# Kernel tuning notes

Hardware: AMD Instinct MI355X
Metric: run time of the kernel (lower is better)

The kernel has to match this reference:

```python
import jax, jax.numpy as jnp
import numpy as np
from jax import lax

MAX_W = 4           # max_subword_block_width
DOWNSAMPLE = 2      # downsample_rate


def setup_inputs() -> dict:
    key = jax.random.key(0)
    k1, k2, k3, k4 = jax.random.split(key, 4)
    B, E, L, K = 8, 512, 4096, 5
    x = jax.random.normal(k1, (B, E, L), dtype=jnp.float32)
    conv_w = jax.random.normal(k2, (E, E, K), dtype=jnp.float32) * (1.0 / np.sqrt(E * K))
    conv_b = jax.random.normal(k3, (E,), dtype=jnp.float32) * 0.02
    score_w = jax.random.normal(k4, (E,), dtype=jnp.float32) * (1.0 / np.sqrt(E))
    return {"x": x, "conv_w": conv_w, "conv_b": conv_b, "score_w": score_w}


def reference(x, conv_w, conv_b, score_w):
    B, E, L = x.shape  # `length` captured BEFORE conv, as in the torch code
    # pre-GBST conv, VALID padding: length becomes L - K + 1
    y = lax.conv_general_dilated(
        x, conv_w, window_strides=(1,), padding='VALID',
        dimension_numbers=('NCH', 'OIH', 'NCH')) + conv_b[None, :, None]
    L2 = y.shape[-1]
    seqs, scores = [], []
    for w in range(1, MAX_W + 1):
        pad = (-L2) % w
        yp = jnp.pad(y, ((0, 0), (0, 0), (0, pad)))  # zero-pad to multiple of w
        nb = yp.shape[-1] // w
        pooled = yp.reshape(B, E, nb, w).mean(-1)          # avg_pool1d(kernel=w, stride=w)
        sc = jnp.einsum('ben,e->bn', pooled, score_w)      # Linear(E,1,bias=False)
        rs = jnp.repeat(pooled, w, axis=-1)                # repeat_interleave
        rsc = jnp.repeat(sc, w, axis=-1)
        cur = rs.shape[-1]
        if cur < L:  # re-pad with zeros up to the ORIGINAL (pre-conv) length
            rs = jnp.pad(rs, ((0, 0), (0, 0), (0, L - cur)))
            rsc = jnp.pad(rsc, ((0, 0), (0, L - cur)))
        seqs.append(rs[:, :, :L])
        scores.append(rsc[:, :L])
    S = jnp.stack(seqs, axis=-1)                           # [B,E,L,W]
    A = jax.nn.softmax(jnp.stack(scores, axis=-1), axis=-1)  # [B,L,W]
    out = jnp.einsum('belw,blw->bel', S, A)                # softmax-weighted combine
    r = DOWNSAMPLE
    Ld = (L // r) * r
    out = out[:, :, :Ld].reshape(B, E, L // r, r).mean(-1)  # final avg_pool1d
    return out
```

## Files before the change

kernel.cpp:

```cpp
#include <hip/hip_runtime.h>
#include <stdint.h>

#define E_DIM 512
#define L_IN  4096
#define L_OUT 4092
#define KW    5
#define B_DIM 8
#define L2P   4096
#define L_DS  2048
#define LP    4160

typedef __attribute__((ext_vector_type(8))) short short8;
typedef __attribute__((ext_vector_type(4))) float f32x4;

__device__ __forceinline__ unsigned short f2bf(float f) {
    uint32_t u = __float_as_uint(f);
    u += 0x7fffu + ((u >> 16) & 1);
    return (unsigned short)(u >> 16);
}
__device__ __forceinline__ float bf2f(unsigned short h) {
    return __uint_as_float((uint32_t)h << 16);
}

__global__ __launch_bounds__(256)
void xt_kernel(const float* __restrict__ x, unsigned short* __restrict__ Xt)
{
    const int b  = blockIdx.z;
    const int i0 = blockIdx.y * 64;
    const int l0 = blockIdx.x * 64;
    __shared__ float T[64][65];
    const int tid = threadIdx.x;

    const int ir = tid >> 4;
    const int cq = (tid & 15) * 4;
    #pragma unroll
    for (int jj = 0; jj < 4; ++jj) {
        int i = jj * 16 + ir;
        float4 v = make_float4(0.f, 0.f, 0.f, 0.f);
        if (l0 < L_IN)
            v = *reinterpret_cast<const float4*>(
                &x[((size_t)b * E_DIM + i0 + i) * L_IN + l0 + cq]);
        T[i][cq + 0] = v.x; T[i][cq + 1] = v.y;
        T[i][cq + 2] = v.z; T[i][cq + 3] = v.w;
    }
    __syncthreads();
    const int h  = tid & 31;
    const int rq = tid >> 5;
    #pragma unroll
    for (int j = 0; j < 8; ++j) {
        int lr = j * 8 + rq;
        ushort2 o;
        o.x = f2bf(T[2 * h][lr]);
        o.y = f2bf(T[2 * h + 1][lr]);
        *reinterpret_cast<ushort2*>(
            &Xt[((size_t)b * LP + l0 + lr) * E_DIM + i0 + 2 * h]) = o;
    }
}

__global__ __launch_bounds__(256)
void wt_kernel(const float* __restrict__ w, unsigned short* __restrict__ Wt)
{
    int idx = blockIdx.x * 256 + threadIdx.x;
    if (idx >= E_DIM * E_DIM) return;
    #pragma unroll
    for (int k = 0; k < KW; ++k)
        Wt[(size_t)k * E_DIM * E_DIM + idx] = f2bf(w[(size_t)idx * KW + k]);
}

#define XS_ROWS  272
#define XS_BYTES (XS_ROWS * 64)
#define N_XCH    (XS_BYTES / 1024)
#define WS_OFF   XS_BYTES
#define WS_BYTES (5 * 128 * 64)
#define LDS_BYTES (XS_BYTES + WS_BYTES)
#define N_CH     (LDS_BYTES / 1024)

__global__ __launch_bounds__(256, 2)
void conv_mfma(const unsigned short* __restrict__ Xt,
               const unsigned short* __restrict__ Wt,
               const float* __restrict__ bias,
               const float* __restrict__ sw,
               unsigned short* __restrict__ y,
               float* __restrict__ sp)
{
    __shared__ __align__(16) unsigned char lds[LDS_BYTES];
    const int l0 = blockIdx.x * 256;
    const int e0 = blockIdx.y * 128;
    const int b  = blockIdx.z;
    const int tid  = threadIdx.x;
    const int lane = tid & 63;
    const int wv   = tid >> 6;
    const int wr = wv >> 1, wc = wv & 1;
    const int lr = lane & 15, lg = lane >> 4;
    const int ln4r = lane >> 2;
    const int xswz = ((lane & 3) ^ ((lane >> 3) & 3)) * 8;

    const int aBase = WS_OFF + (wr * 64 + lr) * 64
                    + ((lg ^ ((lr >> 1) & 3)) << 4);
    int bBase[KW];
    #pragma unroll
    for (int kt = 0; kt < KW; ++kt)
        bBase[kt] = (wc * 128 + lr + kt) * 64
                  + ((lg ^ (((lr + kt) >> 1) & 3)) << 4);

    f32x4 acc[4][8] = {};

    for (int ks = 0; ks < 16; ++ks) {
        const int i0 = ks * 32;
        __syncthreads();
        for (int cch = wv; cch < N_CH; cch += 4) {
            void* lp = (void*)(lds + cch * 1024);
            const unsigned short* gp;
            if (cch < N_XCH) {
                int row = cch * 16 + ln4r;
                gp = Xt + ((size_t)b * LP + l0 + row) * E_DIM + i0 + xswz;
            } else {
                int rk = (cch - N_XCH) * 16 + ln4r;
                int k = rk >> 7, er = rk & 127;
                gp = Wt + ((size_t)k * E_DIM + e0 + er) * E_DIM + i0 + xswz;
            }
            __builtin_amdgcn_global_load_lds(
                (const __attribute__((address_space(1))) void*)gp,
                (__attribute__((address_space(3))) void*)lp,
                16, 0, 0);
        }
        __syncthreads();
        #pragma unroll
        for (int kt = 0; kt < KW; ++kt) {
            short8 aF[4], bF[8];
            #pragma unroll
            for (int m = 0; m < 4; ++m)
                aF[m] = *reinterpret_cast<const short8*>(
                    &lds[aBase + (kt * 128 + m * 16) * 64]);
            #pragma unroll
            for (int n = 0; n < 8; ++n)
                bF[n] = *reinterpret_cast<const short8*>(
                    &lds[bBase[kt] + n * 1024]);
            #pragma unroll
            for (int m = 0; m < 4; ++m)
                #pragma unroll
                for (int n = 0; n < 8; ++n)
                    acc[m][n] = __builtin_amdgcn_mfma_f32_16x16x32_bf16(
                        aF[m], bF[n], acc[m][n], 0, 0, 0);
        }
    }

    float spn[8] = {};
    #pragma unroll
    for (int m = 0; m < 4; ++m)
        #pragma unroll
        for (int q = 0; q < 4; ++q) {
            int e = e0 + wr * 64 + m * 16 + lg * 4 + q;
            float bv = bias[e];
            float wv_s = sw[e];
            unsigned short* yr =
                y + ((size_t)b * E_DIM + e) * L2P + l0 + wc * 128 + lr;
            #pragma unroll
            for (int n = 0; n < 8; ++n) {
                float v = acc[m][n][q] + bv;
                yr[n * 16] = f2bf(v);
                spn[n] = fmaf(v, wv_s, spn[n]);
            }
        }
    #pragma unroll
    for (int n = 0; n < 8; ++n) {
        float p = spn[n];
        p += __shfl_xor(p, 16);
        p += __shfl_xor(p, 32);
        if (lane < 16) {
            int l = l0 + wc * 128 + n * 16 + lane;
            sp[((size_t)b * L2P + l) * 8 + blockIdx.y * 2 + wr] = p;
        }
    }
}

__global__ __launch_bounds__(256)
void weight_kernel(const float* __restrict__ sp, float* __restrict__ A)
{
    const int b  = blockIdx.y;
    const int l0 = blockIdx.x * 256;
    const int tid = threadIdx.x;
    __shared__ float sl[260];

    for (int idx = tid; idx < 260; idx += 256) {
        int l = l0 - 2 + idx;
        float v = 0.f;
        if (l >= 0 && l < L_OUT) {
            const float* p = &sp[((size_t)b * L2P + l) * 8];
            v = ((p[0] + p[1]) + (p[2] + p[3])) + ((p[4] + p[5]) + (p[6] + p[7]));
        }
        sl[idx] = v;
    }
    __syncthreads();

    const int l = l0 + tid;
    if (l >= L_OUT) return;
    #define SL(i) sl[(i) - (l0 - 2)]
    float sc0 = SL(l);
    int n2 = l & ~1;
    float sc1 = 0.5f * (SL(n2) + SL(n2 + 1));
    int n3 = (l / 3) * 3;
    float sc2 = (1.f / 3.f) * (SL(n3) + SL(n3 + 1) + SL(n3 + 2));
    int n4 = l & ~3;
    float sc3 = 0.25f * (SL(n4) + SL(n4 + 1) + SL(n4 + 2) + SL(n4 + 3));
    #undef SL

    float m  = fmaxf(fmaxf(sc0, sc1), fmaxf(sc2, sc3));
    float e0 = __expf(sc0 - m), e1 = __expf(sc1 - m);
    float e2 = __expf(sc2 - m), e3 = __expf(sc3 - m);
    float inv = 1.f / (e0 + e1 + e2 + e3);

    float4 av = make_float4(e0 * inv, e1 * inv, e2 * inv, e3 * inv);
    *reinterpret_cast<float4*>(&A[((size_t)b * L2P + l) * 4]) = av;
}

typedef __attribute__((ext_vector_type(8))) unsigned short u16x8;

__global__ __launch_bounds__(256)
void combine_kernel(const unsigned short* __restrict__ y,
                    const float* __restrict__ A, float* __restrict__ out)
{
    const int e = blockIdx.x;
    const int b = blockIdx.y;
    const int tid = threadIdx.x;
    __shared__ float ys[L2P];

    const unsigned short* yrow = y + ((size_t)b * E_DIM + e) * L2P;
    #pragma unroll
    for (int j = 0; j < 2; ++j) {
        int base = (tid + j * 256) * 8;
        u16x8 v = *reinterpret_cast<const u16x8*>(&yrow[base]);
        #pragma unroll
        for (int t = 0; t < 8; ++t) ys[base + t] = bf2f(v[t]);
    }
    __syncthreads();

    const float* Ab = A + (size_t)b * L2P * 4;
    float* orow = out + ((size_t)b * E_DIM + e) * L_DS;
    #pragma unroll
    for (int j = 0; j < 8; ++j) {
        int m = tid + j * 256;
        float acc = 0.f;
        #pragma unroll
        for (int r = 0; r < 2; ++r) {
            int l = 2 * m + r;
            if (l < L_OUT) {
                const float4 a4 = *reinterpret_cast<const float4*>(&Ab[l * 4]);
                float t = a4.x * ys[l];
                int n2 = l & ~1;
                t += a4.y * 0.5f * (ys[n2] + ys[n2 + 1]);
                int n3 = (l / 3) * 3;
                t += a4.z * (1.f / 3.f) * (ys[n3] + ys[n3 + 1] + ys[n3 + 2]);
                int n4 = l & ~3;
                t += a4.w * 0.25f * (ys[n4] + ys[n4 + 1] + ys[n4 + 2] + ys[n4 + 3]);
                acc += t;
            }
        }
        orow[m] = 0.5f * acc;
    }
}

extern "C" void kernel_launch(void* const* d_in, const int* in_sizes, int n_in,
                              void* d_out, int out_size, void* d_ws, size_t ws_size,
                              hipStream_t stream)
{
    const float* x  = (const float*)d_in[0];
    const float* w  = (const float*)d_in[1];
    const float* bb = (const float*)d_in[2];
    const float* sw = (const float*)d_in[3];
    float* out = (float*)d_out;

    unsigned short* Y = (unsigned short*)d_ws;
    float* SP = (float*)(Y + (size_t)B_DIM * E_DIM * L2P);
    float* A  = SP + (size_t)B_DIM * L2P * 8;
    unsigned short* Xt = (unsigned short*)(A + (size_t)B_DIM * L2P * 4);
    unsigned short* Wt = Xt + (size_t)B_DIM * LP * E_DIM;

    xt_kernel<<<dim3(LP / 64, E_DIM / 64, B_DIM), 256, 0, stream>>>(x, Xt);
    wt_kernel<<<dim3(E_DIM * E_DIM / 256), 256, 0, stream>>>(w, Wt);
    conv_mfma<<<dim3(L2P / 256, E_DIM / 128, B_DIM), 256, 0, stream>>>(Xt, Wt, bb, sw, Y, SP);
    weight_kernel<<<dim3(L2P / 256, B_DIM), 256, 0, stream>>>(SP, A);
    combine_kernel<<<dim3(E_DIM, B_DIM), 256, 0, stream>>>(Y, A, out);
}
```

Before: 118.0 us.

## Double-buffer X tile in LDS to overlap global loads with MFMA compute

The activation tile is split into two LDS buffers, and the next K-slice of X is prefetched with global_load_lds while MFMAs run on the current buffer. Weights stay single-buffered and are reloaded after a barrier at the end of each iteration. The goal is to hide global-to-LDS latency behind compute. The cost is extra LDS (about 17 KB), which may cut occupancy below 2 blocks per CU, and the weight load is still serialized.

After: 119.7 us. About the same (+1.4%).

```diff
diff --git a/kernel.cpp b/kernel.cpp
--- a/kernel.cpp
+++ b/kernel.cpp
@@ -67,13 +67,12 @@
         Wt[(size_t)k * E_DIM * E_DIM + idx] = f2bf(w[(size_t)idx * KW + k]);
 }
 
-#define XS_ROWS  272
-#define XS_BYTES (XS_ROWS * 64)
-#define N_XCH    (XS_BYTES / 1024)
-#define WS_OFF   XS_BYTES
+#define XB_BYTES 17408
+#define N_XCH    (XB_BYTES / 1024)
+#define WOFF     (2 * XB_BYTES)
 #define WS_BYTES (5 * 128 * 64)
-#define LDS_BYTES (XS_BYTES + WS_BYTES)
-#define N_CH     (LDS_BYTES / 1024)
+#define N_WCH    (WS_BYTES / 1024)
+#define LDS_BYTES (WOFF + WS_BYTES)
 
 __global__ __launch_bounds__(256, 2)
 void conv_mfma(const unsigned short* __restrict__ Xt,
@@ -95,7 +94,7 @@
     const int ln4r = lane >> 2;
     const int xswz = ((lane & 3) ^ ((lane >> 3) & 3)) * 8;
 
-    const int aBase = WS_OFF + (wr * 64 + lr) * 64
+    const int aBase = WOFF + (wr * 64 + lr) * 64
                     + ((lg ^ ((lr >> 1) & 3)) << 4);
     int bBase[KW];
     #pragma unroll
@@ -103,28 +102,43 @@
         bBase[kt] = (wc * 128 + lr + kt) * 64
                   + ((lg ^ (((lr + kt) >> 1) & 3)) << 4);
 
-    f32x4 acc[4][8] = {};
-
-    for (int ks = 0; ks < 16; ++ks) {
-        const int i0 = ks * 32;
-        __syncthreads();
-        for (int cch = wv; cch < N_CH; cch += 4) {
-            void* lp = (void*)(lds + cch * 1024);
-            const unsigned short* gp;
-            if (cch < N_XCH) {
-                int row = cch * 16 + ln4r;
-                gp = Xt + ((size_t)b * LP + l0 + row) * E_DIM + i0 + xswz;
-            } else {
-                int rk = (cch - N_XCH) * 16 + ln4r;
-                int k = rk >> 7, er = rk & 127;
-                gp = Wt + ((size_t)k * E_DIM + e0 + er) * E_DIM + i0 + xswz;
-            }
+    const unsigned short* xt_base =
+        Xt + ((size_t)b * LP + l0) * E_DIM + xswz;
+
+    auto stageX = [&](int buf, int i0) {
+        for (int cch = wv; cch < N_XCH; cch += 4) {
+            int row = cch * 16 + ln4r;
+            const unsigned short* gp = xt_base + (size_t)row * E_DIM + i0;
             __builtin_amdgcn_global_load_lds(
                 (const __attribute__((address_space(1))) void*)gp,
-                (__attribute__((address_space(3))) void*)lp,
+                (__attribute__((address_space(3))) void*)(lds + buf * XB_BYTES + cch * 1024),
                 16, 0, 0);
         }
-        __syncthreads();
+    };
+    auto stageW = [&](int i0) {
+        for (int cch = wv; cch < N_WCH; cch += 4) {
+            int rk = cch * 16 + ln4r;
+            int k = rk >> 7, er = rk & 127;
+            const unsigned short* gp =
+                Wt + ((size_t)k * E_DIM + e0 + er) * E_DIM + i0 + xswz;
+            __builtin_amdgcn_global_load_lds(
+                (const __attribute__((address_space(1))) void*)gp,
+                (__attribute__((address_space(3))) void*)(lds + WOFF + cch * 1024),
+                16, 0, 0);
+        }
+    };
+
+    f32x4 acc[4][8] = {};
+
+    stageX(0, 0);
+    stageW(0);
+    asm volatile("s_waitcnt vmcnt(0)" ::: "memory");
+    __builtin_amdgcn_s_barrier();
+
+    for (int ks = 0; ks < 16; ++ks) {
+        const int par = ks & 1;
+        if (ks < 15) stageX(par ^ 1, (ks + 1) * 32);
+
         #pragma unroll
         for (int kt = 0; kt < KW; ++kt) {
             short8 aF[4], bF[8];
@@ -135,13 +149,20 @@
             #pragma unroll
             for (int n = 0; n < 8; ++n)
                 bF[n] = *reinterpret_cast<const short8*>(
-                    &lds[bBase[kt] + n * 1024]);
+                    &lds[par * XB_BYTES + bBase[kt] + n * 1024]);
             #pragma unroll
             for (int m = 0; m < 4; ++m)
                 #pragma unroll
                 for (int n = 0; n < 8; ++n)
                     acc[m][n] = __builtin_amdgcn_mfma_f32_16x16x32_bf16(
                         aF[m], bF[n], acc[m][n], 0, 0, 0);
+        }
+
+        if (ks < 15) {
+            __builtin_amdgcn_s_barrier();
+            stageW((ks + 1) * 32);
+            asm volatile("s_waitcnt vmcnt(0)" ::: "memory");
+            __builtin_amdgcn_s_barrier();
         }
     }
 
```
